# Optimization experiments

Hardware: AMD Instinct MI355X
Metric: run time of the kernel (lower is better)

The kernel has to match this reference:

```python
import jax, jax.numpy as jnp
import numpy as np

NUM_GROUPS = 32
EPS = 1e-6


def group_norm(x, scale, bias):
    # x: [b, c, l]
    b, c, l = x.shape
    xg = x.reshape(b, NUM_GROUPS, (c // NUM_GROUPS) * l)
    mean = jnp.mean(xg, axis=2, keepdims=True)
    var = jnp.var(xg, axis=2, keepdims=True)
    xn = ((xg - mean) * jax.lax.rsqrt(var + EPS)).reshape(b, c, l)
    return xn * scale[None, :, None] + bias[None, :, None]


def conv1x1(x, w, b):
    # pointwise conv: w [out_c, in_c], x [b, in_c, l]
    return jnp.einsum('oc,bcl->bol', w, x) + b[None, :, None]


def setup_inputs() -> dict:
    key = jax.random.key(0)
    ks = jax.random.split(key, 11)
    b, c, l = 4, 512, 4096
    s = 1.0 / np.sqrt(c)
    return {
        'x': jax.random.normal(ks[0], (b, c, l), jnp.float32),
        'gn_scale': jnp.ones((c,), jnp.float32),
        'gn_bias': jnp.zeros((c,), jnp.float32),
        'wq': jax.random.normal(ks[1], (c, c), jnp.float32) * s,
        'bq': jnp.zeros((c,), jnp.float32),
        'wk': jax.random.normal(ks[2], (c, c), jnp.float32) * s,
        'bk': jnp.zeros((c,), jnp.float32),
        'wv': jax.random.normal(ks[3], (c, c), jnp.float32) * s,
        'bv': jnp.zeros((c,), jnp.float32),
        'wp': jax.random.normal(ks[4], (c, c), jnp.float32) * s,
        'bp': jnp.zeros((c,), jnp.float32),
    }


def reference(x, gn_scale, gn_bias, wq, bq, wk, bk, wv, bv, wp, bp):
    h_ = group_norm(x, gn_scale, gn_bias)
    q = conv1x1(h_, wq, bq)  # [b, c, l]
    k = conv1x1(h_, wk, bk)
    v = conv1x1(h_, wv, bv)
    c = q.shape[1]
    # scores w[b,i,j] = sum_c q[b,c,i] k[b,c,j] * c^-0.5, softmax over j
    w = jnp.einsum('bci,bcj->bij', q, k) * (c ** -0.5)
    w = jax.nn.softmax(w, axis=2)
    # out[b,c,i] = sum_j w[b,i,j] v[b,c,j]
    h_ = jnp.einsum('bij,bcj->bci', w, v)
    h_ = conv1x1(h_, wp, bp)
    return x + h_
```

## Files before the change

### kernel.cpp

```cpp
#include <hip/hip_runtime.h>
#include <math.h>

#define BB 4
#define CC 512
#define LL 4096
#define NG 32
#define CPG 16
#define EPSV 1e-6f

typedef short s16x8 __attribute__((ext_vector_type(8)));
typedef __bf16 bf8v __attribute__((ext_vector_type(8)));
typedef float f32x4 __attribute__((ext_vector_type(4)));
typedef unsigned short u16;
typedef unsigned char u8;

typedef const __attribute__((address_space(1))) void g1_void;
typedef __attribute__((address_space(3))) void l3_void;

#define ASM_SBAR() asm volatile("s_barrier" ::: "memory")
#define ASM_WAITV(N) asm volatile("s_waitcnt vmcnt(" #N ")" ::: "memory")

static __device__ __forceinline__ float bf2f(u16 h) {
    unsigned int u = ((unsigned int)h) << 16;
    union { unsigned int u; float f; } c; c.u = u; return c.f;
}
static __device__ __forceinline__ u16 f2bf(float f) {
    union { float f; unsigned int u; } c; c.f = f;
    unsigned int lsb = (c.u >> 16) & 1u;
    c.u += 0x7fffu + lsb;
    return (u16)(c.u >> 16);
}
static __device__ __forceinline__ u8 f2fp8(float f) {
    int v = __builtin_amdgcn_cvt_pk_fp8_f32(f, f, 0, false);
    return (u8)(v & 0xff);
}
static __device__ __forceinline__ bf8v ld_bf8(const u16* p) {
    return *reinterpret_cast<const bf8v*>(p);
}
static __device__ __forceinline__ void gload16(const u16* g, u16* l) {
    __builtin_amdgcn_global_load_lds((g1_void*)g, (l3_void*)l, 16, 0, 0);
}
static __device__ __forceinline__ void gload16b(const u8* g, u8* l) {
    __builtin_amdgcn_global_load_lds((g1_void*)g, (l3_void*)l, 16, 0, 0);
}

__global__ __launch_bounds__(256) void wconv_kernel(const float* __restrict__ w0,
                                                    const float* __restrict__ w1,
                                                    const float* __restrict__ w2,
                                                    const float* __restrict__ w3,
                                                    u16* __restrict__ wbf) {
    int i = blockIdx.x * 256 + threadIdx.x;
    int wsel = blockIdx.y;
    const float* src = (wsel == 0) ? w0 : (wsel == 1) ? w1 : (wsel == 2) ? w2 : w3;
    float4 v = reinterpret_cast<const float4*>(src)[i];
    ushort4 o;
    o.x = f2bf(v.x); o.y = f2bf(v.y); o.z = f2bf(v.z); o.w = f2bf(v.w);
    reinterpret_cast<ushort4*>(wbf + (size_t)wsel * CC * CC)[i] = o;
}

__global__ __launch_bounds__(256) void biascat_kernel(const float* __restrict__ bq,
                                                      const float* __restrict__ bk,
                                                      const float* __restrict__ bv,
                                                      float* __restrict__ bcat,
                                                      float* __restrict__ rowsum) {
    int i = blockIdx.x * 256 + threadIdx.x;
    if (i < 3 * CC) {
        float v = (i < CC) ? bq[i] : (i < 2 * CC ? bk[i - CC] : bv[i - 2 * CC]);
        bcat[i] = v;
    }
    if (i < BB * LL) rowsum[i] = 0.f;
}

__global__ __launch_bounds__(256) void gn_stats_kernel(const float* __restrict__ x,
                                                       float2* __restrict__ stats) {
    int g = blockIdx.x, b = blockIdx.y, t = threadIdx.x;
    const float4* xp = reinterpret_cast<const float4*>(x + ((size_t)b * CC + (size_t)g * CPG) * LL);
    float s = 0.f, ss = 0.f;
    for (int it = 0; it < 64; ++it) {
        float4 v = xp[it * 256 + t];
        s += v.x + v.y + v.z + v.w;
        ss += v.x * v.x + v.y * v.y + v.z * v.z + v.w * v.w;
    }
    #pragma unroll
    for (int off = 32; off; off >>= 1) { s += __shfl_xor(s, off, 64); ss += __shfl_xor(ss, off, 64); }
    __shared__ float rs[4], rss[4];
    int wave = t >> 6, lane = t & 63;
    if (lane == 0) { rs[wave] = s; rss[wave] = ss; }
    __syncthreads();
    if (t == 0) {
        float S = rs[0] + rs[1] + rs[2] + rs[3];
        float SS = rss[0] + rss[1] + rss[2] + rss[3];
        float mean = S * (1.f / 65536.f);
        float var = SS * (1.f / 65536.f) - mean * mean;
        var = fmaxf(var, 0.f);
        stats[b * NG + g] = make_float2(mean, rsqrtf(var + EPSV));
    }
}

__global__ __launch_bounds__(256) void gn_norm_t_kernel(const float* __restrict__ x,
                                                        const float2* __restrict__ stats,
                                                        const float* __restrict__ gsc,
                                                        const float* __restrict__ gbi,
                                                        u16* __restrict__ hT) {
    int lt = blockIdx.x, ct = blockIdx.y, b = blockIdx.z;
    __shared__ u16 tile[64][72];
    int t = threadIdx.x;
    int cl0 = t >> 4, c4 = (t & 15) * 4;
    #pragma unroll
    for (int p = 0; p < 4; ++p) {
        int cl = p * 16 + cl0;
        int cg = ct * 64 + cl;
        float2 st = stats[b * NG + (cg >> 4)];
        float sc = gsc[cg] * st.y;
        float bi = gbi[cg];
        float4 v = *reinterpret_cast<const float4*>(x + ((size_t)b * CC + cg) * LL + lt * 64 + c4);
        tile[cl][c4 + 0] = f2bf((v.x - st.x) * sc + bi);
        tile[cl][c4 + 1] = f2bf((v.y - st.x) * sc + bi);
        tile[cl][c4 + 2] = f2bf((v.z - st.x) * sc + bi);
        tile[cl][c4 + 3] = f2bf((v.w - st.x) * sc + bi);
    }
    __syncthreads();
    int r = t >> 3, c8 = (t & 7) * 8;
    #pragma unroll
    for (int p = 0; p < 2; ++p) {
        int ll = p * 32 + r;
        s16x8 ov;
        #pragma unroll
        for (int j = 0; j < 8; ++j) ov[j] = (short)tile[c8 + j][ll];
        u16* hp = hT + ((size_t)b * LL + lt * 64 + ll) * CC + ct * 64 + c8;
        *reinterpret_cast<s16x8*>(hp) = ov;
    }
}

template <int MODE>
__global__ __launch_bounds__(256) void gemm_kernel(const u16* __restrict__ A, size_t asb, int lda,
                                                   const u16* __restrict__ B, size_t bsb, int ldb,
                                                   const float* __restrict__ bias,
                                                   u8* __restrict__ Oq, u8* __restrict__ Ok,
                                                   u8* __restrict__ Ov, size_t osb,
                                                   const float* __restrict__ xres,
                                                   float* __restrict__ fout, int K) {
    __shared__ u16 pool[17408];
    u8* pool8 = (u8*)pool;
    int mt = blockIdx.x, nt = blockIdx.y, b = blockIdx.z;
    int t = threadIdx.x;
    int wave = t >> 6, lane = t & 63;
    int wm = (wave >> 1) * 64, wn = (wave & 1) * 64;
    int l15 = lane & 15, quad = lane >> 4;
    f32x4 acc[4][4] = {};
    const u16* Ab = A + (size_t)b * asb + (size_t)mt * 128 * lda;
    const u16* Bb = B + (size_t)b * bsb + (size_t)nt * 128 * ldb;
    int swzg = ((lane & 3) ^ ((lane >> 2) & 3) ^ ((lane >> 4) & 3)) * 8;
    int row0 = wave * 16 + (lane >> 2);
    int row1 = 64 + row0;
    const u16* Ap0 = Ab + (size_t)row0 * lda + swzg;
    const u16* Ap1 = Ab + (size_t)row1 * lda + swzg;
    const u16* Bp0 = Bb + (size_t)row0 * ldb + swzg;
    const u16* Bp1 = Bb + (size_t)row1 * ldb + swzg;
    int wo = wave * 512;
    int swzf = (l15 & 3) ^ (l15 >> 2);
    int aoff = (wm + l15) * 32 + ((quad ^ swzf) * 8);
    int boff = (wn + l15) * 32 + ((quad ^ swzf) * 8);
    const int iters = K >> 5;
    gload16(Ap0, pool + wo);                gload16(Ap1, pool + 2048 + wo);
    gload16(Bp0, pool + 8192 + wo);         gload16(Bp1, pool + 8192 + 2048 + wo);
    gload16(Ap0 + 32, pool + 4096 + wo);    gload16(Ap1 + 32, pool + 4096 + 2048 + wo);
    gload16(Bp0 + 32, pool + 12288 + wo);   gload16(Bp1 + 32, pool + 12288 + 2048 + wo);
    for (int i = 0; i < iters; ++i) {
        if (i + 1 < iters) { ASM_WAITV(4); } else { ASM_WAITV(0); }
        ASM_SBAR();
        int bs = (i & 1) * 4096;
        const u16* As = pool + bs;
        const u16* Bs = pool + 8192 + bs;
        bf8v af[4], bfr[4];
        #pragma unroll
        for (int ii = 0; ii < 4; ++ii)
            af[ii] = ld_bf8(&As[aoff + ii * 512]);
        #pragma unroll
        for (int j = 0; j < 4; ++j)
            bfr[j] = ld_bf8(&Bs[boff + j * 512]);
        #pragma unroll
        for (int ii = 0; ii < 4; ++ii)
            #pragma unroll
            for (int j = 0; j < 4; ++j)
                acc[ii][j] = __builtin_amdgcn_mfma_f32_16x16x32_bf16(af[ii], bfr[j], acc[ii][j], 0, 0, 0);
        ASM_SBAR();
        if (i + 2 < iters) {
            int kk = (i + 2) * 32;
            u16* as = pool + bs; u16* bsp = pool + 8192 + bs;
            gload16(Ap0 + kk, as + wo);        gload16(Ap1 + kk, as + 2048 + wo);
            gload16(Bp0 + kk, bsp + wo);       gload16(Bp1 + kk, bsp + 2048 + wo);
        }
    }
    if (MODE == 0) {
        int nt_sel = nt >> 2, ntl = nt & 3;
        if (nt_sel == 2) {
            __syncthreads();
            #pragma unroll
            for (int j = 0; j < 4; ++j) {
                float bv = bias[nt * 128 + wn + j * 16 + l15];
                #pragma unroll
                for (int i = 0; i < 4; ++i) {
                    int col = wn + j * 16 + l15;
                    int row = wm + i * 16 + quad * 4;
                    unsigned int w = __builtin_amdgcn_cvt_pk_fp8_f32(acc[i][j][0] + bv, acc[i][j][1] + bv, 0, false);
                    w = __builtin_amdgcn_cvt_pk_fp8_f32(acc[i][j][2] + bv, acc[i][j][3] + bv, w, true);
                    *reinterpret_cast<unsigned int*>(&pool8[col * 144 + row]) = w;
                }
            }
            __syncthreads();
            u8* Ob = Ov + (size_t)b * osb + (size_t)(ntl * 128) * LL + mt * 128;
            #pragma unroll
            for (int it = 0; it < 4; ++it) {
                int idx = it * 256 + t;
                int row = idx >> 3, ch = (idx & 7) * 16;
                *reinterpret_cast<float4*>(Ob + (size_t)row * LL + ch) =
                    *reinterpret_cast<const float4*>(&pool8[row * 144 + ch]);
            }
        } else {
            u8* Oc = (nt_sel == 0 ? Oq : Ok) + (size_t)b * osb
                     + (size_t)(mt * 128) * CC + ntl * 128 + wn + l15;
            #pragma unroll
            for (int j = 0; j < 4; ++j) {
                float bv = bias[nt * 128 + wn + j * 16 + l15];
                #pragma unroll
                for (int i = 0; i < 4; ++i)
                    #pragma unroll
                    for (int r = 0; r < 4; ++r) {
                        int row = wm + i * 16 + quad * 4 + r;
                        Oc[(size_t)row * CC + j * 16] = f2fp8(acc[i][j][r] + bv);
                    }
            }
        }
    } else {
        __syncthreads();
        #pragma unroll
        for (int j = 0; j < 4; ++j) {
            float bv = bias[nt * 128 + wn + j * 16 + l15];
            #pragma unroll
            for (int i = 0; i < 4; ++i)
                #pragma unroll
                for (int r = 0; r < 4; ++r) {
                    int row = wm + i * 16 + quad * 4 + r;
                    int col = wn + j * 16 + l15;
                    pool[col * 136 + row] = f2bf(acc[i][j][r] + bv);
                }
        }
        __syncthreads();
        const float* xb = xres + ((size_t)b * CC + nt * 128) * LL + mt * 128;
        float* ob = fout + ((size_t)b * CC + nt * 128) * LL + mt * 128;
        #pragma unroll
        for (int it = 0; it < 16; ++it) {
            int idx = it * 256 + t;
            int cl = idx >> 5, ch = (idx & 31) * 4;
            short4 pv = *reinterpret_cast<const short4*>(&pool[cl * 136 + ch]);
            float4 xv = *reinterpret_cast<const float4*>(xb + (size_t)cl * LL + ch);
            float4 ov;
            ov.x = xv.x + bf2f((u16)pv.x);
            ov.y = xv.y + bf2f((u16)pv.y);
            ov.z = xv.z + bf2f((u16)pv.z);
            ov.w = xv.w + bf2f((u16)pv.w);
            *reinterpret_cast<float4*>(ob + (size_t)cl * LL + ch) = ov;
        }
    }
}

template <int MODE>
__global__ __launch_bounds__(256) void gemm8_kernel(const u8* __restrict__ A, size_t asb, int lda,
                                                    const u8* __restrict__ B, size_t bsb, int ldb,
                                                    float scale,
                                                    u8* __restrict__ Out8, u16* __restrict__ OutH,
                                                    size_t osb, int Nout, int K,
                                                    float* __restrict__ rsum) {
    __shared__ u8 pool8[MODE == 1 ? 32768 : 34816];
    int mt = blockIdx.x, nt = blockIdx.y, b = blockIdx.z;
    int t = threadIdx.x;
    int wave = t >> 6, lane = t & 63;
    int wm = (wave >> 1) * 64, wn = (wave & 1) * 64;
    int l15 = lane & 15, quad = lane >> 4;
    f32x4 acc[4][4] = {};
    int R = wave * 32 + (lane >> 1);
    int c16 = ((lane & 1) ^ (R & 1) ^ ((R >> 2) & 1)) * 16;
    const u8* Ap = A + (size_t)b * asb + (size_t)(mt * 128 + R) * lda + c16;
    const u8* Bp = B + (size_t)b * bsb + (size_t)(nt * 128 + R) * ldb + c16;
    int wo = wave * 1024;
    int p = (l15 & 1) ^ ((l15 >> 2) & 1);
    int fo = (((quad >> 1) ^ p) * 16) + (quad & 1) * 8;
    int abase = (wm + l15) * 32 + fo;
    int bbase = (wn + l15) * 32 + fo;
    const int iters = K >> 6;
    #define STG(ii, bsv) do { int kk = (ii) * 64;                          \
        gload16b(Ap + kk,      pool8 + (bsv) + wo);                        \
        gload16b(Ap + kk + 32, pool8 + (bsv) + 4096 + wo);                 \
        gload16b(Bp + kk,      pool8 + 16384 + (bsv) + wo);                \
        gload16b(Bp + kk + 32, pool8 + 16384 + (bsv) + 4096 + wo); } while (0)
    STG(0, 0);
    STG(1, 8192);
    for (int i = 0; i < iters; ++i) {
        if (i + 1 < iters) { ASM_WAITV(4); } else { ASM_WAITV(0); }
        ASM_SBAR();
        int bs = (i & 1) * 8192;
        const u8* As = pool8 + bs;
        const u8* Bs = pool8 + 16384 + bs;
        #pragma unroll
        for (int h = 0; h < 2; ++h) {
            long af[4], bfr[4];
            #pragma unroll
            for (int ii = 0; ii < 4; ++ii)
                af[ii] = *reinterpret_cast<const long*>(As + h * 4096 + abase + ii * 512);
            #pragma unroll
            for (int j = 0; j < 4; ++j)
                bfr[j] = *reinterpret_cast<const long*>(Bs + h * 4096 + bbase + j * 512);
            #pragma unroll
            for (int ii = 0; ii < 4; ++ii)
                #pragma unroll
                for (int j = 0; j < 4; ++j)
                    acc[ii][j] = __builtin_amdgcn_mfma_f32_16x16x32_fp8_fp8(af[ii], bfr[j], acc[ii][j], 0, 0, 0);
        }
        ASM_SBAR();
        if (i + 2 < iters) STG(i + 2, bs);
    }
    #undef STG
    if (MODE == 1) {
        u8* Ob = Out8 + (size_t)b * osb + (size_t)(mt * 128) * Nout + nt * 128 + wn + l15;
        #pragma unroll
        for (int i = 0; i < 4; ++i) {
            #pragma unroll
            for (int r = 0; r < 4; ++r) {
                int row = wm + i * 16 + quad * 4 + r;
                u8* rp = Ob + (size_t)row * Nout;
                float part = 0.f;
                #pragma unroll
                for (int j = 0; j < 4; ++j) {
                    float v = __expf(acc[i][j][r] * scale - 3.0f);
                    part += v;
                    rp[j * 16] = f2fp8(v);
                }
                part += __shfl_xor(part, 1, 64);
                part += __shfl_xor(part, 2, 64);
                part += __shfl_xor(part, 4, 64);
                part += __shfl_xor(part, 8, 64);
                if (l15 == 0)
                    atomicAdd(rsum + (size_t)b * LL + mt * 128 + row, part);
            }
        }
    } else {
        __syncthreads();
        u16* poolh = (u16*)pool8;
        float invl[4][4];
        #pragma unroll
        for (int i = 0; i < 4; ++i)
            #pragma unroll
            for (int r = 0; r < 4; ++r)
                invl[i][r] = 1.f / rsum[(size_t)b * LL + mt * 128 + wm + i * 16 + quad * 4 + r];
        #pragma unroll
        for (int j = 0; j < 4; ++j)
            #pragma unroll
            for (int i = 0; i < 4; ++i)
                #pragma unroll
                for (int r = 0; r < 4; ++r) {
                    int row = wm + i * 16 + quad * 4 + r;
                    int col = wn + j * 16 + l15;
                    poolh[row * 136 + col] = f2bf(acc[i][j][r] * invl[i][r]);
                }
        __syncthreads();
        u16* Ob = OutH + (size_t)b * osb + (size_t)(mt * 128) * Nout + nt * 128;
        #pragma unroll
        for (int it = 0; it < 8; ++it) {
            int idx = it * 256 + t;
            int row = idx >> 4, ch = (idx & 15) * 8;
            s16x8 val = *reinterpret_cast<const s16x8*>(&poolh[row * 136 + ch]);
            *reinterpret_cast<s16x8*>(Ob + (size_t)row * Nout + ch) = val;
        }
    }
}

extern "C" void kernel_launch(void* const* d_in, const int* in_sizes, int n_in,
                              void* d_out, int out_size, void* d_ws, size_t ws_size,
                              hipStream_t stream) {
    const float* x   = (const float*)d_in[0];
    const float* gsc = (const float*)d_in[1];
    const float* gbi = (const float*)d_in[2];
    const float* wq  = (const float*)d_in[3];
    const float* bq  = (const float*)d_in[4];
    const float* wk  = (const float*)d_in[5];
    const float* bk  = (const float*)d_in[6];
    const float* wv  = (const float*)d_in[7];
    const float* bv  = (const float*)d_in[8];
    const float* wp  = (const float*)d_in[9];
    const float* bp  = (const float*)d_in[10];
    float* out = (float*)d_out;

    char* ws = (char*)d_ws;
    const size_t SZ   = (size_t)BB * LL * CC * 2;
    const size_t QSZ  = (size_t)BB * LL * CC;
    const size_t WQSZ = (size_t)4 * CC * CC * 2;
    const size_t RSZ  = (size_t)BB * LL * 4;
    u16* bufA = (u16*)(ws);
    u8*  q8   = (u8*)(ws + SZ);
    u8*  k8   = (u8*)(ws + SZ + QSZ);
    u8*  v8   = (u8*)(ws + SZ + 2 * QSZ);
    u16* wbf  = (u16*)(ws + SZ + 3 * QSZ);
    float2* stats = (float2*)(ws + SZ + 3 * QSZ + WQSZ);
    float* bcat   = (float*)(ws + SZ + 3 * QSZ + WQSZ + 4096);
    float* rowsum = (float*)(ws + SZ + 3 * QSZ + WQSZ + 4096 + 8192);
    u8* S8 = (u8*)(ws + SZ + 3 * QSZ + WQSZ + 4096 + 8192 + RSZ);
    const float scale = 0.044194173824159216f;
    const size_t BLC = (size_t)LL * CC;

    wconv_kernel<<<dim3(256, 4), 256, 0, stream>>>(wq, wk, wv, wp, wbf);
    biascat_kernel<<<dim3(64), 256, 0, stream>>>(bq, bk, bv, bcat, rowsum);
    gn_stats_kernel<<<dim3(NG, BB), 256, 0, stream>>>(x, stats);
    gn_norm_t_kernel<<<dim3(64, 8, BB), 256, 0, stream>>>(x, stats, gsc, gbi, bufA);
    gemm_kernel<0><<<dim3(32, 12, BB), 256, 0, stream>>>(bufA, BLC, CC, wbf, 0, CC, bcat,
                                                         q8, k8, v8, BLC, nullptr, nullptr, CC);
    gemm8_kernel<1><<<dim3(32, 32, BB), 256, 0, stream>>>(q8, BLC, CC, k8, BLC, CC, scale,
                                                          S8, nullptr, (size_t)LL * LL, LL, CC, rowsum);
    gemm8_kernel<2><<<dim3(32, 4, BB), 256, 0, stream>>>(S8, (size_t)LL * LL, LL, v8, BLC, LL, 1.f,
                                                         nullptr, bufA, BLC, CC, LL, rowsum);
    gemm_kernel<3><<<dim3(32, 4, BB), 256, 0, stream>>>(bufA, BLC, CC, wbf + 3 * CC * CC, 0, CC,
                                                        bp, nullptr, nullptr, nullptr, 0, x, out, CC);
}
```

Baseline: 310.9 us.

## Triple-buffer LDS in GEMM kernels to drop the second barrier per iteration

Both the bf16 and fp8 GEMM main loops move from two LDS stages to three rotating stages. The prefetch for iteration i+2 is now issued right after the fragment reads, before the MFMAs, which removes the trailing barrier in each iteration. MFMA sections are wrapped in s_setprio to favour matrix issue. The fp8 kernel also loads both K-halves of fragments at once and hoists the rsum reciprocal loads before the main loop. Larger LDS footprints (48KB) may reduce occupancy.

```diff
diff --git a/kernel.cpp b/kernel.cpp
--- a/kernel.cpp
+++ b/kernel.cpp
@@ -140,7 +140,7 @@
                                                    u8* __restrict__ Ov, size_t osb,
                                                    const float* __restrict__ xres,
                                                    float* __restrict__ fout, int K) {
-    __shared__ u16 pool[17408];
+    __shared__ u16 pool[24576];
     u8* pool8 = (u8*)pool;
     int mt = blockIdx.x, nt = blockIdx.y, b = blockIdx.z;
     int t = threadIdx.x;
@@ -163,15 +163,15 @@
     int boff = (wn + l15) * 32 + ((quad ^ swzf) * 8);
     const int iters = K >> 5;
     gload16(Ap0, pool + wo);                gload16(Ap1, pool + 2048 + wo);
-    gload16(Bp0, pool + 8192 + wo);         gload16(Bp1, pool + 8192 + 2048 + wo);
+    gload16(Bp0, pool + 12288 + wo);        gload16(Bp1, pool + 12288 + 2048 + wo);
     gload16(Ap0 + 32, pool + 4096 + wo);    gload16(Ap1 + 32, pool + 4096 + 2048 + wo);
-    gload16(Bp0 + 32, pool + 12288 + wo);   gload16(Bp1 + 32, pool + 12288 + 2048 + wo);
+    gload16(Bp0 + 32, pool + 16384 + wo);   gload16(Bp1 + 32, pool + 16384 + 2048 + wo);
+    int bs = 0;
     for (int i = 0; i < iters; ++i) {
         if (i + 1 < iters) { ASM_WAITV(4); } else { ASM_WAITV(0); }
         ASM_SBAR();
-        int bs = (i & 1) * 4096;
         const u16* As = pool + bs;
-        const u16* Bs = pool + 8192 + bs;
+        const u16* Bs = pool + 12288 + bs;
         bf8v af[4], bfr[4];
         #pragma unroll
         for (int ii = 0; ii < 4; ++ii)
@@ -179,18 +179,21 @@
         #pragma unroll
         for (int j = 0; j < 4; ++j)
             bfr[j] = ld_bf8(&Bs[boff + j * 512]);
+        if (i + 2 < iters) {
+            int kk = (i + 2) * 32;
+            int nb = bs + 8192; if (nb >= 12288) nb -= 12288;
+            u16* as = pool + nb; u16* bsp = pool + 12288 + nb;
+            gload16(Ap0 + kk, as + wo);        gload16(Ap1 + kk, as + 2048 + wo);
+            gload16(Bp0 + kk, bsp + wo);       gload16(Bp1 + kk, bsp + 2048 + wo);
+        }
+        __builtin_amdgcn_s_setprio(1);
         #pragma unroll
         for (int ii = 0; ii < 4; ++ii)
             #pragma unroll
             for (int j = 0; j < 4; ++j)
                 acc[ii][j] = __builtin_amdgcn_mfma_f32_16x16x32_bf16(af[ii], bfr[j], acc[ii][j], 0, 0, 0);
-        ASM_SBAR();
-        if (i + 2 < iters) {
-            int kk = (i + 2) * 32;
-            u16* as = pool + bs; u16* bsp = pool + 8192 + bs;
-            gload16(Ap0 + kk, as + wo);        gload16(Ap1 + kk, as + 2048 + wo);
-            gload16(Bp0 + kk, bsp + wo);       gload16(Bp1 + kk, bsp + 2048 + wo);
-        }
+        __builtin_amdgcn_s_setprio(0);
+        bs += 4096; if (bs >= 12288) bs -= 12288;
     }
     if (MODE == 0) {
         int nt_sel = nt >> 2, ntl = nt & 3;
@@ -272,7 +275,7 @@
                                                     u8* __restrict__ Out8, u16* __restrict__ OutH,
                                                     size_t osb, int Nout, int K,
                                                     float* __restrict__ rsum) {
-    __shared__ u8 pool8[MODE == 1 ? 32768 : 34816];
+    __shared__ u8 pool8[49152];
     int mt = blockIdx.x, nt = blockIdx.y, b = blockIdx.z;
     int t = threadIdx.x;
     int wave = t >> 6, lane = t & 63;
@@ -292,33 +295,52 @@
     #define STG(ii, bsv) do { int kk = (ii) * 64;                          \
         gload16b(Ap + kk,      pool8 + (bsv) + wo);                        \
         gload16b(Ap + kk + 32, pool8 + (bsv) + 4096 + wo);                 \
-        gload16b(Bp + kk,      pool8 + 16384 + (bsv) + wo);                \
-        gload16b(Bp + kk + 32, pool8 + 16384 + (bsv) + 4096 + wo); } while (0)
+        gload16b(Bp + kk,      pool8 + 24576 + (bsv) + wo);                \
+        gload16b(Bp + kk + 32, pool8 + 24576 + (bsv) + 4096 + wo); } while (0)
+    float invl[4][4];
+    if (MODE == 2) {
+        #pragma unroll
+        for (int i = 0; i < 4; ++i)
+            #pragma unroll
+            for (int r = 0; r < 4; ++r)
+                invl[i][r] = 1.f / rsum[(size_t)b * LL + mt * 128 + wm + i * 16 + quad * 4 + r];
+    }
     STG(0, 0);
     STG(1, 8192);
+    int bs = 0;
     for (int i = 0; i < iters; ++i) {
         if (i + 1 < iters) { ASM_WAITV(4); } else { ASM_WAITV(0); }
         ASM_SBAR();
-        int bs = (i & 1) * 8192;
         const u8* As = pool8 + bs;
-        const u8* Bs = pool8 + 16384 + bs;
-        #pragma unroll
-        for (int h = 0; h < 2; ++h) {
-            long af[4], bfr[4];
-            #pragma unroll
-            for (int ii = 0; ii < 4; ++ii)
-                af[ii] = *reinterpret_cast<const long*>(As + h * 4096 + abase + ii * 512);
+        const u8* Bs = pool8 + 24576 + bs;
+        long af0[4], bf0[4], af1[4], bf1[4];
+        #pragma unroll
+        for (int ii = 0; ii < 4; ++ii) {
+            af0[ii] = *reinterpret_cast<const long*>(As + abase + ii * 512);
+            af1[ii] = *reinterpret_cast<const long*>(As + 4096 + abase + ii * 512);
+        }
+        #pragma unroll
+        for (int j = 0; j < 4; ++j) {
+            bf0[j] = *reinterpret_cast<const long*>(Bs + bbase + j * 512);
+            bf1[j] = *reinterpret_cast<const long*>(Bs + 4096 + bbase + j * 512);
+        }
+        if (i + 2 < iters) {
+            int nb = bs + 16384; if (nb >= 24576) nb -= 24576;
+            STG(i + 2, nb);
+        }
+        __builtin_amdgcn_s_setprio(1);
+        #pragma unroll
+        for (int ii = 0; ii < 4; ++ii)
             #pragma unroll
             for (int j = 0; j < 4; ++j)
-                bfr[j] = *reinterpret_cast<const long*>(Bs + h * 4096 + bbase + j * 512);
-            #pragma unroll
-            for (int ii = 0; ii < 4; ++ii)
-                #pragma unroll
-                for (int j = 0; j < 4; ++j)
-                    acc[ii][j] = __builtin_amdgcn_mfma_f32_16x16x32_fp8_fp8(af[ii], bfr[j], acc[ii][j], 0, 0, 0);
-        }
-        ASM_SBAR();
-        if (i + 2 < iters) STG(i + 2, bs);
+                acc[ii][j] = __builtin_amdgcn_mfma_f32_16x16x32_fp8_fp8(af0[ii], bf0[j], acc[ii][j], 0, 0, 0);
+        #pragma unroll
+        for (int ii = 0; ii < 4; ++ii)
+            #pragma unroll
+            for (int j = 0; j < 4; ++j)
+                acc[ii][j] = __builtin_amdgcn_mfma_f32_16x16x32_fp8_fp8(af1[ii], bf1[j], acc[ii][j], 0, 0, 0);
+        __builtin_amdgcn_s_setprio(0);
+        bs += 8192; if (bs >= 24576) bs -= 24576;
     }
     #undef STG
     if (MODE == 1) {
@@ -347,12 +369,6 @@
     } else {
         __syncthreads();
         u16* poolh = (u16*)pool8;
-        float invl[4][4];
-        #pragma unroll
-        for (int i = 0; i < 4; ++i)
-            #pragma unroll
-            for (int r = 0; r < 4; ++r)
-                invl[i][r] = 1.f / rsum[(size_t)b * LL + mt * 128 + wm + i * 16 + quad * 4 + r];
         #pragma unroll
         for (int j = 0; j < 4; ++j)
             #pragma unroll
```

Result: no change. 305.8 us (-1.7%).
